# Optimization experiments

Measured on AMD Instinct MI355X. Metric: run time of the kernel, lower is better.

## Reference

```python
import jax, jax.numpy as jnp
import numpy as np

ALPHA = 0.2  # LeakyReLU negative slope
NEG_INF = -1e12


def setup_inputs() -> dict:
    key = jax.random.key(0)
    k1, k2, k3, k4 = jax.random.split(key, 4)
    B, N, F_in, F_out = 8, 4096, 128, 64
    inp = jax.random.normal(k1, (B, N, F_in), dtype=jnp.float32)
    adj = jax.random.randint(k2, (B, N, N), 0, 2, dtype=jnp.int32)
    # xavier-uniform-ish init for W, a
    W = jax.random.normal(k3, (F_in, F_out), dtype=jnp.float32) * (2.0 / (F_in + F_out)) ** 0.5
    a = jax.random.normal(k4, (2 * F_out, 1), dtype=jnp.float32) * (2.0 / (2 * F_out + 1)) ** 0.5
    return {"inp": inp, "adj": adj, "W": W, "a": a}


def reference(inp, adj, W, a):
    # inp: [B,N,F_in], adj: [B,N,N] int, W: [F_in,F_out], a: [2*F_out,1]
    F_out = W.shape[1]
    h = jnp.einsum('bnf,fo->bno', inp, W)          # [B,N,F_out]
    a1 = a[:F_out, 0]                              # [F_out]
    a2 = a[F_out:, 0]                              # [F_out]
    # e[b,i,j] = leakyrelu(h_i . a1 + h_j . a2)  (== concat([h_i,h_j]) @ a)
    s1 = h @ a1                                    # [B,N]
    s2 = h @ a2                                    # [B,N]
    e = s1[:, :, None] + s2[:, None, :]            # [B,N,N]
    e = jnp.where(e > 0, e, ALPHA * e)             # LeakyReLU
    att = jnp.where(adj > 0, e, NEG_INF)
    att = jax.nn.softmax(att, axis=-1)             # [B,N,N]
    # dropout p=0.0 -> identity
    h_prime = jnp.einsum('bij,bjo->bio', att, h)   # [B,N,F_out]
    return jax.nn.elu(h_prime)
```

## Files before the change

kernel.cpp:

```cpp
#include <hip/hip_runtime.h>
#include <hip/hip_bf16.h>
#include <cstdint>

typedef __attribute__((ext_vector_type(8))) short short8;
typedef __attribute__((ext_vector_type(4))) float floatx4;

#define LEAKY_ALPHA 0.2f

__device__ __forceinline__ unsigned short f2bf_rne(float f) {
    unsigned u = __float_as_uint(f);
    unsigned r = u + 0x7FFFu + ((u >> 16) & 1u);
    return (unsigned short)(r >> 16);
}

__global__ __launch_bounds__(256) void k_h(const float* __restrict__ inp,
                                           const float* __restrict__ W,
                                           const float* __restrict__ a,
                                           unsigned short* __restrict__ hT,
                                           float* __restrict__ s1,
                                           float* __restrict__ s2) {
    __shared__ float hs[64][65];
    const int tid  = threadIdx.x;
    const int wv   = tid >> 6;
    const int lane = tid & 63;
    const int blk  = blockIdx.x;
    const int b     = blk >> 6;
    const int ibase = (blk & 63) * 64;

    const float a1 = a[lane];
    const float a2 = a[64 + lane];

    for (int rr = 0; rr < 16; ++rr) {
        const int rloc = wv * 16 + rr;
        const int row  = ibase + rloc;
        const float* ip = inp + ((size_t)(b * 4096 + row)) * 128;
        float acc = 0.f;
        #pragma unroll
        for (int f = 0; f < 128; f += 4) {
            float4 v = *(const float4*)(ip + f);
            acc += v.x * W[(f + 0) * 64 + lane];
            acc += v.y * W[(f + 1) * 64 + lane];
            acc += v.z * W[(f + 2) * 64 + lane];
            acc += v.w * W[(f + 3) * 64 + lane];
        }
        hs[rloc][lane] = acc;
        float r1 = acc * a1;
        float r2 = acc * a2;
        #pragma unroll
        for (int off = 32; off > 0; off >>= 1) {
            r1 += __shfl_xor(r1, off);
            r2 += __shfl_xor(r2, off);
        }
        if (lane == 0) {
            s1[b * 4096 + row] = r1;
            s2[b * 4096 + row] = r2;
        }
    }
    __syncthreads();

    const int n  = tid >> 2;
    const int iq = tid & 3;
    unsigned pk[8];
    #pragma unroll
    for (int s = 0; s < 16; s += 2) {
        unsigned lo = f2bf_rne(hs[iq * 16 + s    ][n]);
        unsigned hi = f2bf_rne(hs[iq * 16 + s + 1][n]);
        pk[s >> 1] = lo | (hi << 16);
    }
    unsigned short* dst = hT + ((size_t)(b * 64 + n)) * 4096 + ibase + iq * 16;
    *(int4*)(dst)     = *(int4*)&pk[0];
    *(int4*)(dst + 8) = *(int4*)&pk[4];
}

__global__ __launch_bounds__(256, 4) void k_attn(const int* __restrict__ adj,
                                                 const unsigned short* __restrict__ hT,
                                                 const float* __restrict__ s1g,
                                                 const float* __restrict__ s2g,
                                                 float* __restrict__ out) {
    __shared__ float s2s[4096];
    __shared__ float accbuf[2][64][17];
    __shared__ float lbuf[2][64];

    const int tid   = threadIdx.x;
    const int b     = blockIdx.x >> 7;
    const int rtile = blockIdx.x & 127;

    {
        const float* src = s2g + b * 4096;
        #pragma unroll
        for (int t = 0; t < 4; ++t) {
            int idx = tid * 16 + t * 4;
            *(float4*)&s2s[idx] = *(const float4*)(src + idx);
        }
    }
    __syncthreads();

    const int wv    = tid >> 6;
    const int lane  = tid & 63;
    const int jhalf = wv >> 1;
    const int m     = lane & 15;
    const int kh    = lane >> 4;
    const int rbase = rtile * 32 + (wv & 1) * 16;
    const int row   = rbase + m;

    const float s1v = s1g[b * 4096 + row];
    const int jb0 = jhalf * 2048 + kh * 8;
    const int* adjrow = adj + ((size_t)(b * 4096 + row)) * 4096 + jb0;
    const unsigned short* hrow0 = hT + ((size_t)(b * 64 +  0 + m)) * 4096 + jb0;
    const unsigned short* hrow1 = hT + ((size_t)(b * 64 + 16 + m)) * 4096 + jb0;
    const unsigned short* hrow2 = hT + ((size_t)(b * 64 + 32 + m)) * 4096 + jb0;
    const unsigned short* hrow3 = hT + ((size_t)(b * 64 + 48 + m)) * 4096 + jb0;

    floatx4 acc0 = (floatx4){0.f,0.f,0.f,0.f};
    floatx4 acc1 = (floatx4){0.f,0.f,0.f,0.f};
    floatx4 acc2 = (floatx4){0.f,0.f,0.f,0.f};
    floatx4 acc3 = (floatx4){0.f,0.f,0.f,0.f};
    float lsum = 0.f;

    int4   ra0_0, ra1_0, ra0_1, ra1_1;
    short8 rb0_0, rb1_0, rb2_0, rb3_0, rb0_1, rb1_1, rb2_1, rb3_1;

    ra0_0 = *(const int4*)(adjrow);        ra1_0 = *(const int4*)(adjrow + 4);
    rb0_0 = *(const short8*)(hrow0);       rb1_0 = *(const short8*)(hrow1);
    rb2_0 = *(const short8*)(hrow2);       rb3_0 = *(const short8*)(hrow3);
    ra0_1 = *(const int4*)(adjrow + 32);   ra1_1 = *(const int4*)(adjrow + 36);
    rb0_1 = *(const short8*)(hrow0 + 32);  rb1_1 = *(const short8*)(hrow1 + 32);
    rb2_1 = *(const short8*)(hrow2 + 32);  rb3_1 = *(const short8*)(hrow3 + 32);

#define GAT_STEP(SL, STEPIDX)                                                  \
    do {                                                                       \
        const int4   ca0 = ra0_##SL, ca1 = ra1_##SL;                           \
        const short8 cb0 = rb0_##SL, cb1 = rb1_##SL;                           \
        const short8 cb2 = rb2_##SL, cb3 = rb3_##SL;                           \
        const int poff = (((STEPIDX) + 2) & 63) * 32;   \
        ra0_##SL = *(const int4*)(adjrow + poff);                              \
        ra1_##SL = *(const int4*)(adjrow + poff + 4);                          \
        rb0_##SL = *(const short8*)(hrow0 + poff);                             \
        rb1_##SL = *(const short8*)(hrow1 + poff);                             \
        rb2_##SL = *(const short8*)(hrow2 + poff);                             \
        rb3_##SL = *(const short8*)(hrow3 + poff);                             \
        const int soff = jb0 + (STEPIDX) * 32;                                 \
        const float4 csa = *(const float4*)&s2s[soff];                         \
        const float4 csb = *(const float4*)&s2s[soff + 4];                     \
        const int   av[8] = {ca0.x, ca0.y, ca0.z, ca0.w,                       \
                             ca1.x, ca1.y, ca1.z, ca1.w};                      \
        const float sv[8] = {csa.x, csa.y, csa.z, csa.w,                       \
                             csb.x, csb.y, csb.z, csb.w};                      \
        short8 af;                                                             \
        float psum = 0.f;                                                      \
        _Pragma("unroll")                                                      \
        for (int t = 0; t < 8; ++t) {                                          \
            float e = s1v + sv[t];                                             \
            e = fmaxf(e, LEAKY_ALPHA * e);                                     \
            float pv = (av[t] > 0) ? __expf(e) : 0.f;                          \
            psum += pv;                                                        \
            af[t] = (short)f2bf_rne(pv);                                       \
        }                                                                      \
        lsum += psum;                                                          \
        acc0 = __builtin_amdgcn_mfma_f32_16x16x32_bf16(af, cb0, acc0, 0,0,0);  \
        acc1 = __builtin_amdgcn_mfma_f32_16x16x32_bf16(af, cb1, acc1, 0,0,0);  \
        acc2 = __builtin_amdgcn_mfma_f32_16x16x32_bf16(af, cb2, acc2, 0,0,0);  \
        acc3 = __builtin_amdgcn_mfma_f32_16x16x32_bf16(af, cb3, acc3, 0,0,0);  \
    } while (0)

    #pragma unroll 1
    for (int it = 0; it < 32; ++it) {
        const int s0 = it * 2;
        GAT_STEP(0, s0);
        GAT_STEP(1, s0 + 1);
    }
#undef GAT_STEP

    lsum += __shfl_xor(lsum, 16);
    lsum += __shfl_xor(lsum, 32);

    floatx4 accs[4] = {acc0, acc1, acc2, acc3};

    if (wv >= 2) {
        #pragma unroll
        for (int f = 0; f < 4; ++f)
            #pragma unroll
            for (int r = 0; r < 4; ++r)
                accbuf[wv - 2][lane][f * 4 + r] = accs[f][r];
        lbuf[wv - 2][lane] = lsum;
    }
    __syncthreads();
    if (wv < 2) {
        const float ltot = lsum + lbuf[wv][lane];
        #pragma unroll
        for (int f = 0; f < 4; ++f) {
            #pragma unroll
            for (int r = 0; r < 4; ++r) {
                float v = accs[f][r] + accbuf[wv][lane][f * 4 + r];
                const int drow = (lane >> 4) * 4 + r;
                const float lr = __shfl(ltot, drow);
                const float hp = v / lr;
                const float o  = (hp > 0.f) ? hp : (__expf(hp) - 1.f);
                out[((size_t)(b * 4096 + rbase + drow)) * 64 + f * 16 + (lane & 15)] = o;
            }
        }
    }
}

extern "C" void kernel_launch(void* const* d_in, const int* in_sizes, int n_in,
                              void* d_out, int out_size, void* d_ws, size_t ws_size,
                              hipStream_t stream) {
    const float* inp = (const float*)d_in[0];
    const int*   adj = (const int*)d_in[1];
    const float* W   = (const float*)d_in[2];
    const float* a   = (const float*)d_in[3];
    float* out = (float*)d_out;

    unsigned short* hT = (unsigned short*)d_ws;
    float* s1 = (float*)((char*)d_ws + (size_t)8 * 64 * 4096 * 2);
    float* s2 = s1 + 8 * 4096;

    k_h<<<512, 256, 0, stream>>>(inp, W, a, hT, s1, s2);
    k_attn<<<1024, 256, 0, stream>>>(adj, hT, s1, s2, out);
}
```

Before: 902.2 us.

## Pack adjacency into bitmask in a pre-pass and consume bits in attention kernel

Adds a separate kernel that reads the int32 adjacency matrix once and packs each run of 32 entries into a 32-bit mask. The attention kernel then loads one mask word per step instead of two int4 adjacency loads and tests bits. The adjacency is still read in full by the pack kernel, so total traffic does not fall. The gain, if any, has to come from the extra launch and mask write costing less than the adjacency stalls inside the MFMA loop.

Result: no change. 892.4 us (-1.1%).

```diff
diff --git a/kernel.cpp b/kernel.cpp
--- a/kernel.cpp
+++ b/kernel.cpp
@@ -11,6 +11,22 @@
     unsigned u = __float_as_uint(f);
     unsigned r = u + 0x7FFFu + ((u >> 16) & 1u);
     return (unsigned short)(r >> 16);
+}
+
+__global__ __launch_bounds__(256) void k_pack(const int* __restrict__ adj,
+                                              unsigned* __restrict__ mask) {
+    const size_t t = (size_t)blockIdx.x * 256 + threadIdx.x;
+    const int* p = adj + t * 32;
+    unsigned m = 0;
+    #pragma unroll
+    for (int k = 0; k < 8; ++k) {
+        const int4 v = *(const int4*)(p + k * 4);
+        m |= (v.x > 0 ? 1u : 0u) << (k * 4 + 0);
+        m |= (v.y > 0 ? 1u : 0u) << (k * 4 + 1);
+        m |= (v.z > 0 ? 1u : 0u) << (k * 4 + 2);
+        m |= (v.w > 0 ? 1u : 0u) << (k * 4 + 3);
+    }
+    mask[t] = m;
 }
 
 __global__ __launch_bounds__(256) void k_h(const float* __restrict__ inp,
@@ -72,7 +88,7 @@
     *(int4*)(dst + 8) = *(int4*)&pk[4];
 }
 
-__global__ __launch_bounds__(256, 4) void k_attn(const int* __restrict__ adj,
+__global__ __launch_bounds__(256, 4) void k_attn(const unsigned* __restrict__ mask,
                                                  const unsigned short* __restrict__ hT,
                                                  const float* __restrict__ s1g,
                                                  const float* __restrict__ s2g,
@@ -105,7 +121,7 @@
 
     const float s1v = s1g[b * 4096 + row];
     const int jb0 = jhalf * 2048 + kh * 8;
-    const int* adjrow = adj + ((size_t)(b * 4096 + row)) * 4096 + jb0;
+    const unsigned* mrow = mask + ((size_t)(b * 4096 + row)) * 128 + jhalf * 64;
     const unsigned short* hrow0 = hT + ((size_t)(b * 64 +  0 + m)) * 4096 + jb0;
     const unsigned short* hrow1 = hT + ((size_t)(b * 64 + 16 + m)) * 4096 + jb0;
     const unsigned short* hrow2 = hT + ((size_t)(b * 64 + 32 + m)) * 4096 + jb0;
@@ -117,24 +133,24 @@
     floatx4 acc3 = (floatx4){0.f,0.f,0.f,0.f};
     float lsum = 0.f;
 
-    int4   ra0_0, ra1_0, ra0_1, ra1_1;
+    unsigned rm_0, rm_1;
     short8 rb0_0, rb1_0, rb2_0, rb3_0, rb0_1, rb1_1, rb2_1, rb3_1;
 
-    ra0_0 = *(const int4*)(adjrow);        ra1_0 = *(const int4*)(adjrow + 4);
+    rm_0  = mrow[0];
     rb0_0 = *(const short8*)(hrow0);       rb1_0 = *(const short8*)(hrow1);
     rb2_0 = *(const short8*)(hrow2);       rb3_0 = *(const short8*)(hrow3);
-    ra0_1 = *(const int4*)(adjrow + 32);   ra1_1 = *(const int4*)(adjrow + 36);
+    rm_1  = mrow[1];
     rb0_1 = *(const short8*)(hrow0 + 32);  rb1_1 = *(const short8*)(hrow1 + 32);
     rb2_1 = *(const short8*)(hrow2 + 32);  rb3_1 = *(const short8*)(hrow3 + 32);
 
 #define GAT_STEP(SL, STEPIDX)                                                  \
     do {                                                                       \
-        const int4   ca0 = ra0_##SL, ca1 = ra1_##SL;                           \
+        const unsigned cmw = rm_##SL;                                          \
         const short8 cb0 = rb0_##SL, cb1 = rb1_##SL;                           \
         const short8 cb2 = rb2_##SL, cb3 = rb3_##SL;                           \
-        const int poff = (((STEPIDX) + 2) & 63) * 32;   \
-        ra0_##SL = *(const int4*)(adjrow + poff);                              \
-        ra1_##SL = *(const int4*)(adjrow + poff + 4);                          \
+        const int pstep = ((STEPIDX) + 2) & 63;         \
+        const int poff = pstep * 32;                                           \
+        rm_##SL  = mrow[pstep];                                                \
         rb0_##SL = *(const short8*)(hrow0 + poff);                             \
         rb1_##SL = *(const short8*)(hrow1 + poff);                             \
         rb2_##SL = *(const short8*)(hrow2 + poff);                             \
@@ -142,8 +158,7 @@
         const int soff = jb0 + (STEPIDX) * 32;                                 \
         const float4 csa = *(const float4*)&s2s[soff];                         \
         const float4 csb = *(const float4*)&s2s[soff + 4];                     \
-        const int   av[8] = {ca0.x, ca0.y, ca0.z, ca0.w,                       \
-                             ca1.x, ca1.y, ca1.z, ca1.w};                      \
+        const unsigned mb = (cmw >> (kh * 8)) & 0xffu;                         \
         const float sv[8] = {csa.x, csa.y, csa.z, csa.w,                       \
                              csb.x, csb.y, csb.z, csb.w};                      \
         short8 af;                                                             \
@@ -152,7 +167,7 @@
         for (int t = 0; t < 8; ++t) {                                          \
             float e = s1v + sv[t];                                             \
             e = fmaxf(e, LEAKY_ALPHA * e);                                     \
-            float pv = (av[t] > 0) ? __expf(e) : 0.f;                          \
+            float pv = ((mb >> t) & 1u) ? __expf(e) : 0.f;                     \
             psum += pv;                                                        \
             af[t] = (short)f2bf_rne(pv);                                       \
         }                                                                      \
@@ -214,7 +229,9 @@
     unsigned short* hT = (unsigned short*)d_ws;
     float* s1 = (float*)((char*)d_ws + (size_t)8 * 64 * 4096 * 2);
     float* s2 = s1 + 8 * 4096;
-
+    unsigned* mask = (unsigned*)(s2 + 8 * 4096);
+
+    k_pack<<<16384, 256, 0, stream>>>(adj, mask);
     k_h<<<512, 256, 0, stream>>>(inp, W, a, hT, s1, s2);
-    k_attn<<<1024, 256, 0, stream>>>(adj, hT, s1, s2, out);
-}
+    k_attn<<<1024, 256, 0, stream>>>(mask, hT, s1, s2, out);
+}
```
